# Kernel tuning notes

Measured on AMD Instinct MI355X. Metric: run time of the kernel, lower is better.

Reference implementation:

```python
import jax, jax.numpy as jnp
import numpy as np

N = 50000   # nodes
E = 600000  # edges
D = 128     # input_dim
H = 128     # hidden_dim
K = 2       # num_layers (propagation hops)


def setup_inputs() -> dict:
    key = jax.random.key(0)
    k1, k2, k3 = jax.random.split(key, 3)
    x = jax.random.normal(k1, (N, D), dtype=jnp.float32)
    edge_index = jax.random.randint(k2, (2, E), 0, N, dtype=jnp.int64)
    # Linear(input_dim -> hidden_dim) params (PyG default: glorot-ish weight, zero bias)
    W = jax.random.normal(k3, (H, D), dtype=jnp.float32) / np.float32(np.sqrt(D))
    b = jnp.zeros((H,), dtype=jnp.float32)
    return {"x": x, "edge_index": edge_index, "W": W, "b": b}


def reference(x, edge_index, W, b):
    n = x.shape[0]
    loop = jnp.arange(n, dtype=edge_index.dtype)
    # gcn_norm: add self-loops with weight 1, symmetric normalization
    row = jnp.concatenate([edge_index[0], loop])  # source nodes
    col = jnp.concatenate([edge_index[1], loop])  # target nodes
    w = jnp.ones(row.shape[0], dtype=x.dtype)
    deg = jax.ops.segment_sum(w, col, num_segments=n)
    dinv = jnp.where(deg > 0, jax.lax.rsqrt(deg), jnp.zeros_like(deg))
    norm = dinv[row] * w * dinv[col]  # [E+N]
    # K hops of normalized sparse propagation: x <- A_hat @ x
    for _ in range(K):
        x = jax.ops.segment_sum(norm[:, None] * x[row], col, num_segments=n)
    # Linear projection + activation
    z = x @ W.T + b
    return jax.nn.relu(z)
```

## Files before the change

### kernel.cpp

```cpp
#include <hip/hip_runtime.h>

#define D 128
#define CAP 128
typedef unsigned int uint;
typedef unsigned short ushort;
typedef __attribute__((ext_vector_type(8))) short bf16x8;
typedef __attribute__((ext_vector_type(4))) float f32x4;

__device__ __forceinline__ float2 bf2_to_f2(uint v) {
    union { uint u; float f; } a, b;
    a.u = v << 16;
    b.u = v & 0xffff0000u;
    return make_float2(a.f, b.f);
}
__device__ __forceinline__ uint f2_to_bf2(float x, float y) {
    uint xu = __float_as_uint(x), yu = __float_as_uint(y);
    xu += 0x7fffu + ((xu >> 16) & 1u);
    yu += 0x7fffu + ((yu >> 16) & 1u);
    return (xu >> 16) | (yu & 0xffff0000u);
}

__global__ __launch_bounds__(256) void build_cast_kernel(
        const int* __restrict__ ei, int E, int* __restrict__ deg, int* __restrict__ slots,
        const float* __restrict__ x, uint2* __restrict__ zX, int n,
        const float* __restrict__ W, uint* __restrict__ Wbf,
        int cntB, int xB) {
    int b = blockIdx.x, t = threadIdx.x;
    if (b < cntB) {
        int e = b * 256 + t;
        if (e < E) {
            int r = ei[e];
            int c = ei[E + e];
            int pos = atomicAdd(&deg[c], 1);
            if (pos < CAP) slots[c * CAP + pos] = r;
        }
    } else if (b < cntB + xB) {
        int idx = (b - cntB) * 256 + t;
        if (idx < n * 32) {
            float4 v = ((const float4*)x)[idx];
            uint2 o;
            o.x = f2_to_bf2(v.x, v.y);
            o.y = f2_to_bf2(v.z, v.w);
            zX[idx] = o;
        }
    } else {
        int i = (b - cntB - xB) * 256 + t;
        if (i < (D * D) / 2) {
            float2 wv = ((const float2*)W)[i];
            Wbf[i] = f2_to_bf2(wv.x, wv.y);
        }
    }
}

__global__ __launch_bounds__(256) void prop1_kernel(const uint* __restrict__ zin,
                                                    uint* __restrict__ zout,
                                                    const int* __restrict__ deg,
                                                    const int* __restrict__ slots,
                                                    int n) {
    int wv = threadIdx.x >> 6, lane = threadIdx.x & 63;
    int c = blockIdx.x * 4 + wv;
    if (c >= n) return;
    int len = deg[c]; if (len > CAP) len = CAP;
    const int* lst = slots + c * CAP;
    size_t selfoff = (size_t)c * 64 + lane;
    float dc = rsqrtf((float)(len + 1));
    float2 sf = bf2_to_f2(zin[selfoff]);
    float2 acc = make_float2(sf.x * dc, sf.y * dc);
    int k = 0;
    for (; k + 7 < len; k += 8) {
        int r0 = lst[k],     r1 = lst[k + 1], r2 = lst[k + 2], r3 = lst[k + 3];
        int r4 = lst[k + 4], r5 = lst[k + 5], r6 = lst[k + 6], r7 = lst[k + 7];
        uint v0 = zin[(size_t)r0 * 64 + lane], v1 = zin[(size_t)r1 * 64 + lane];
        uint v2 = zin[(size_t)r2 * 64 + lane], v3 = zin[(size_t)r3 * 64 + lane];
        uint v4 = zin[(size_t)r4 * 64 + lane], v5 = zin[(size_t)r5 * 64 + lane];
        uint v6 = zin[(size_t)r6 * 64 + lane], v7 = zin[(size_t)r7 * 64 + lane];
        float d0 = rsqrtf((float)(deg[r0] + 1)), d1 = rsqrtf((float)(deg[r1] + 1));
        float d2 = rsqrtf((float)(deg[r2] + 1)), d3 = rsqrtf((float)(deg[r3] + 1));
        float d4 = rsqrtf((float)(deg[r4] + 1)), d5 = rsqrtf((float)(deg[r5] + 1));
        float d6 = rsqrtf((float)(deg[r6] + 1)), d7 = rsqrtf((float)(deg[r7] + 1));
        float2 f0 = bf2_to_f2(v0), f1 = bf2_to_f2(v1), f2 = bf2_to_f2(v2), f3 = bf2_to_f2(v3);
        float2 f4 = bf2_to_f2(v4), f5 = bf2_to_f2(v5), f6 = bf2_to_f2(v6), f7 = bf2_to_f2(v7);
        acc.x += (fmaf(d0, f0.x, d1 * f1.x) + fmaf(d2, f2.x, d3 * f3.x))
               + (fmaf(d4, f4.x, d5 * f5.x) + fmaf(d6, f6.x, d7 * f7.x));
        acc.y += (fmaf(d0, f0.y, d1 * f1.y) + fmaf(d2, f2.y, d3 * f3.y))
               + (fmaf(d4, f4.y, d5 * f5.y) + fmaf(d6, f6.y, d7 * f7.y));
    }
    for (; k < len; ++k) {
        int r = lst[k];
        float d = rsqrtf((float)(deg[r] + 1));
        float2 f = bf2_to_f2(zin[(size_t)r * 64 + lane]);
        acc.x = fmaf(d, f.x, acc.x);
        acc.y = fmaf(d, f.y, acc.y);
    }
    float sc = dc * dc;
    zout[selfoff] = f2_to_bf2(acc.x * sc, acc.y * sc);
}

__global__ __launch_bounds__(256) void prop2_kernel(const uint* __restrict__ zin,
                                                    uint* __restrict__ zout,
                                                    const int* __restrict__ deg,
                                                    const int* __restrict__ slots,
                                                    int n) {
    int wv = threadIdx.x >> 6, lane = threadIdx.x & 63;
    int c = blockIdx.x * 4 + wv;
    if (c >= n) return;
    int len = deg[c]; if (len > CAP) len = CAP;
    const int* lst = slots + c * CAP;
    size_t selfoff = (size_t)c * 64 + lane;
    float2 acc = bf2_to_f2(zin[selfoff]);
    int k = 0;
    for (; k + 7 < len; k += 8) {
        int r0 = lst[k],     r1 = lst[k + 1], r2 = lst[k + 2], r3 = lst[k + 3];
        int r4 = lst[k + 4], r5 = lst[k + 5], r6 = lst[k + 6], r7 = lst[k + 7];
        uint v0 = zin[(size_t)r0 * 64 + lane], v1 = zin[(size_t)r1 * 64 + lane];
        uint v2 = zin[(size_t)r2 * 64 + lane], v3 = zin[(size_t)r3 * 64 + lane];
        uint v4 = zin[(size_t)r4 * 64 + lane], v5 = zin[(size_t)r5 * 64 + lane];
        uint v6 = zin[(size_t)r6 * 64 + lane], v7 = zin[(size_t)r7 * 64 + lane];
        float2 f0 = bf2_to_f2(v0), f1 = bf2_to_f2(v1), f2 = bf2_to_f2(v2), f3 = bf2_to_f2(v3);
        float2 f4 = bf2_to_f2(v4), f5 = bf2_to_f2(v5), f6 = bf2_to_f2(v6), f7 = bf2_to_f2(v7);
        acc.x += ((f0.x + f1.x) + (f2.x + f3.x)) + ((f4.x + f5.x) + (f6.x + f7.x));
        acc.y += ((f0.y + f1.y) + (f2.y + f3.y)) + ((f4.y + f5.y) + (f6.y + f7.y));
    }
    for (; k < len; ++k) {
        float2 f = bf2_to_f2(zin[(size_t)lst[k] * 64 + lane]);
        acc.x += f.x; acc.y += f.y;
    }
    float s = rsqrtf((float)(len + 1));
    zout[selfoff] = f2_to_bf2(acc.x * s, acc.y * s);
}

#define GN 64
__global__ __launch_bounds__(256) void gemm_mfma(const uint4* __restrict__ x2,
                                                 const uint4* __restrict__ Wbf,
                                                 const float* __restrict__ bias,
                                                 float* __restrict__ out, int n) {
    __shared__ __align__(16) ushort xs[GN][136];
    __shared__ __align__(16) ushort ws[D][136];
    int t = threadIdx.x;
    int n0 = blockIdx.x * GN;
    for (int i = t; i < D * 16; i += 256) {
        int row = i >> 4, c8 = i & 15;
        uint4 v = Wbf[i];
        *(uint4*)&ws[row][c8 * 8] = v;
    }
    for (int i = t; i < GN * 16; i += 256) {
        int row = i >> 4, c8 = i & 15;
        int node = n0 + row;
        uint4 v = (node < n) ? x2[(size_t)node * 16 + c8] : make_uint4(0u, 0u, 0u, 0u);
        *(uint4*)&xs[row][c8 * 8] = v;
    }
    __syncthreads();

    int w = t >> 6, lane = t & 63;
    int m0 = w * 16;
    int mrow = lane & 15, quad = lane >> 4;

    bf16x8 a[4];
#pragma unroll
    for (int q = 0; q < 4; ++q)
        a[q] = *(const bf16x8*)&xs[m0 + mrow][q * 32 + quad * 8];

    f32x4 acc[8];
#pragma unroll
    for (int ht = 0; ht < 8; ++ht) {
        acc[ht] = (f32x4){0.f, 0.f, 0.f, 0.f};
#pragma unroll
        for (int q = 0; q < 4; ++q) {
            bf16x8 bfr = *(const bf16x8*)&ws[ht * 16 + mrow][q * 32 + quad * 8];
            acc[ht] = __builtin_amdgcn_mfma_f32_16x16x32_bf16(a[q], bfr, acc[ht], 0, 0, 0);
        }
    }

#pragma unroll
    for (int ht = 0; ht < 8; ++ht) {
        int h = ht * 16 + mrow;
        float bv = bias[h];
#pragma unroll
        for (int reg = 0; reg < 4; ++reg) {
            int node = n0 + m0 + quad * 4 + reg;
            if (node < n)
                out[(size_t)node * D + h] = fmaxf(acc[ht][reg] + bv, 0.f);
        }
    }
}

extern "C" void kernel_launch(void* const* d_in, const int* in_sizes, int n_in,
                              void* d_out, int out_size, void* d_ws, size_t ws_size,
                              hipStream_t stream) {
    const float* x  = (const float*)d_in[0];
    const int*   ei = (const int*)d_in[1];
    const float* W  = (const float*)d_in[2];
    const float* bias = (const float*)d_in[3];
    float* out = (float*)d_out;
    int N = in_sizes[0] / D;
    int E = in_sizes[1] / 2;

    char* p = (char*)d_ws;
    auto alloc = [&](size_t bytes) -> void* {
        void* r = p; p += (bytes + 511) & ~(size_t)511; return r;
    };
    int*    deg     = (int*)alloc((size_t)N * 4);
    int*    slots   = (int*)alloc((size_t)N * CAP * 4);
    uint*   zX      = (uint*)alloc((size_t)N * 64 * 4);
    uint*   zB      = (uint*)alloc((size_t)N * 64 * 4);
    uint*   zA      = (uint*)alloc((size_t)N * 64 * 4);
    uint*   Wbf     = (uint*)alloc((size_t)(D * D / 2) * 4);

    int cntB = (E + 255) / 256;
    int xB   = (N * 32 + 255) / 256;
    int wB   = ((D * D / 2) + 255) / 256;

    hipMemsetAsync(deg, 0, (size_t)N * 4, stream);
    build_cast_kernel<<<cntB + xB + wB, 256, 0, stream>>>(ei, E, deg, slots, x, (uint2*)zX, N,
                                                          W, Wbf, cntB, xB);
    prop1_kernel<<<(N + 3) / 4, 256, 0, stream>>>(zX, zB, deg, slots, N);
    prop2_kernel<<<(N + 3) / 4, 256, 0, stream>>>(zB, zA, deg, slots, N);
    gemm_mfma<<<(N + GN - 1) / GN, 256, 0, stream>>>((const uint4*)zA, (const uint4*)Wbf, bias, out, N);
}
```

Measured before the change: 199.3 us.

## Fuse second propagation hop into MFMA GEMM and shrink neighbor slot capacity

The second propagation hop now runs inside the GEMM kernel. Each wave gathers neighbor features for 16 nodes and writes the bf16 result straight into shared memory, so the intermediate feature buffer is never written to or read back from global memory. The weight cast to bf16 moves into each GEMM block, one prop2 launch is removed, and the per-node slot capacity is halved from 128 to 64 to cut the adjacency footprint. The cost is that far fewer waves now do the latency-bound gather, each handling 16 nodes in series with LDS-limited occupancy, which may hide memory latency worse. Every block also redundantly converts the full weight matrix.

```diff
diff --git a/kernel.cpp b/kernel.cpp
--- a/kernel.cpp
+++ b/kernel.cpp
@@ -1,7 +1,7 @@
 #include <hip/hip_runtime.h>
 
 #define D 128
-#define CAP 128
+#define CAP 64
 typedef unsigned int uint;
 typedef unsigned short ushort;
 typedef __attribute__((ext_vector_type(8))) short bf16x8;
@@ -22,9 +22,7 @@
 
 __global__ __launch_bounds__(256) void build_cast_kernel(
         const int* __restrict__ ei, int E, int* __restrict__ deg, int* __restrict__ slots,
-        const float* __restrict__ x, uint2* __restrict__ zX, int n,
-        const float* __restrict__ W, uint* __restrict__ Wbf,
-        int cntB, int xB) {
+        const float* __restrict__ x, uint2* __restrict__ zX, int n, int cntB) {
     int b = blockIdx.x, t = threadIdx.x;
     if (b < cntB) {
         int e = b * 256 + t;
@@ -34,7 +32,7 @@
             int pos = atomicAdd(&deg[c], 1);
             if (pos < CAP) slots[c * CAP + pos] = r;
         }
-    } else if (b < cntB + xB) {
+    } else {
         int idx = (b - cntB) * 256 + t;
         if (idx < n * 32) {
             float4 v = ((const float4*)x)[idx];
@@ -42,12 +40,6 @@
             o.x = f2_to_bf2(v.x, v.y);
             o.y = f2_to_bf2(v.z, v.w);
             zX[idx] = o;
-        }
-    } else {
-        int i = (b - cntB - xB) * 256 + t;
-        if (i < (D * D) / 2) {
-            float2 wv = ((const float2*)W)[i];
-            Wbf[i] = f2_to_bf2(wv.x, wv.y);
         }
     }
 }
@@ -96,62 +88,55 @@
     zout[selfoff] = f2_to_bf2(acc.x * sc, acc.y * sc);
 }
 
-__global__ __launch_bounds__(256) void prop2_kernel(const uint* __restrict__ zin,
-                                                    uint* __restrict__ zout,
-                                                    const int* __restrict__ deg,
-                                                    const int* __restrict__ slots,
-                                                    int n) {
-    int wv = threadIdx.x >> 6, lane = threadIdx.x & 63;
-    int c = blockIdx.x * 4 + wv;
-    if (c >= n) return;
-    int len = deg[c]; if (len > CAP) len = CAP;
-    const int* lst = slots + c * CAP;
-    size_t selfoff = (size_t)c * 64 + lane;
-    float2 acc = bf2_to_f2(zin[selfoff]);
-    int k = 0;
-    for (; k + 7 < len; k += 8) {
-        int r0 = lst[k],     r1 = lst[k + 1], r2 = lst[k + 2], r3 = lst[k + 3];
-        int r4 = lst[k + 4], r5 = lst[k + 5], r6 = lst[k + 6], r7 = lst[k + 7];
-        uint v0 = zin[(size_t)r0 * 64 + lane], v1 = zin[(size_t)r1 * 64 + lane];
-        uint v2 = zin[(size_t)r2 * 64 + lane], v3 = zin[(size_t)r3 * 64 + lane];
-        uint v4 = zin[(size_t)r4 * 64 + lane], v5 = zin[(size_t)r5 * 64 + lane];
-        uint v6 = zin[(size_t)r6 * 64 + lane], v7 = zin[(size_t)r7 * 64 + lane];
-        float2 f0 = bf2_to_f2(v0), f1 = bf2_to_f2(v1), f2 = bf2_to_f2(v2), f3 = bf2_to_f2(v3);
-        float2 f4 = bf2_to_f2(v4), f5 = bf2_to_f2(v5), f6 = bf2_to_f2(v6), f7 = bf2_to_f2(v7);
-        acc.x += ((f0.x + f1.x) + (f2.x + f3.x)) + ((f4.x + f5.x) + (f6.x + f7.x));
-        acc.y += ((f0.y + f1.y) + (f2.y + f3.y)) + ((f4.y + f5.y) + (f6.y + f7.y));
-    }
-    for (; k < len; ++k) {
-        float2 f = bf2_to_f2(zin[(size_t)lst[k] * 64 + lane]);
-        acc.x += f.x; acc.y += f.y;
-    }
-    float s = rsqrtf((float)(len + 1));
-    zout[selfoff] = f2_to_bf2(acc.x * s, acc.y * s);
-}
-
 #define GN 64
-__global__ __launch_bounds__(256) void gemm_mfma(const uint4* __restrict__ x2,
-                                                 const uint4* __restrict__ Wbf,
-                                                 const float* __restrict__ bias,
-                                                 float* __restrict__ out, int n) {
+__global__ __launch_bounds__(256) void prop2_gemm(const uint* __restrict__ zin,
+                                                  const int* __restrict__ deg,
+                                                  const int* __restrict__ slots,
+                                                  const float* __restrict__ W,
+                                                  const float* __restrict__ bias,
+                                                  float* __restrict__ out, int n) {
     __shared__ __align__(16) ushort xs[GN][136];
     __shared__ __align__(16) ushort ws[D][136];
     int t = threadIdx.x;
+    int w = t >> 6, lane = t & 63;
     int n0 = blockIdx.x * GN;
-    for (int i = t; i < D * 16; i += 256) {
-        int row = i >> 4, c8 = i & 15;
-        uint4 v = Wbf[i];
-        *(uint4*)&ws[row][c8 * 8] = v;
+
+    for (int i = t; i < (D * D) / 2; i += 256) {
+        float2 wv = ((const float2*)W)[i];
+        uint u = f2_to_bf2(wv.x, wv.y);
+        int row = i >> 6, col2 = i & 63;
+        *(uint*)&xs[0][0 * 0];
+        *(uint*)&ws[row][col2 * 2] = u;
     }
-    for (int i = t; i < GN * 16; i += 256) {
-        int row = i >> 4, c8 = i & 15;
-        int node = n0 + row;
-        uint4 v = (node < n) ? x2[(size_t)node * 16 + c8] : make_uint4(0u, 0u, 0u, 0u);
-        *(uint4*)&xs[row][c8 * 8] = v;
+
+    for (int i = 0; i < 16; ++i) {
+        int c = n0 + w * 16 + i;
+        if (c >= n) break;
+        int len = deg[c]; if (len > CAP) len = CAP;
+        const int* lst = slots + c * CAP;
+        float2 acc = bf2_to_f2(zin[(size_t)c * 64 + lane]);
+        int k = 0;
+        for (; k + 7 < len; k += 8) {
+            int r0 = lst[k],     r1 = lst[k + 1], r2 = lst[k + 2], r3 = lst[k + 3];
+            int r4 = lst[k + 4], r5 = lst[k + 5], r6 = lst[k + 6], r7 = lst[k + 7];
+            uint v0 = zin[(size_t)r0 * 64 + lane], v1 = zin[(size_t)r1 * 64 + lane];
+            uint v2 = zin[(size_t)r2 * 64 + lane], v3 = zin[(size_t)r3 * 64 + lane];
+            uint v4 = zin[(size_t)r4 * 64 + lane], v5 = zin[(size_t)r5 * 64 + lane];
+            uint v6 = zin[(size_t)r6 * 64 + lane], v7 = zin[(size_t)r7 * 64 + lane];
+            float2 f0 = bf2_to_f2(v0), f1 = bf2_to_f2(v1), f2 = bf2_to_f2(v2), f3 = bf2_to_f2(v3);
+            float2 f4 = bf2_to_f2(v4), f5 = bf2_to_f2(v5), f6 = bf2_to_f2(v6), f7 = bf2_to_f2(v7);
+            acc.x += ((f0.x + f1.x) + (f2.x + f3.x)) + ((f4.x + f5.x) + (f6.x + f7.x));
+            acc.y += ((f0.y + f1.y) + (f2.y + f3.y)) + ((f4.y + f5.y) + (f6.y + f7.y));
+        }
+        for (; k < len; ++k) {
+            float2 f = bf2_to_f2(zin[(size_t)lst[k] * 64 + lane]);
+            acc.x += f.x; acc.y += f.y;
+        }
+        float s = rsqrtf((float)(len + 1));
+        *(uint*)&xs[w * 16 + i][lane * 2] = f2_to_bf2(acc.x * s, acc.y * s);
     }
     __syncthreads();
 
-    int w = t >> 6, lane = t & 63;
     int m0 = w * 16;
     int mrow = lane & 15, quad = lane >> 4;
 
@@ -203,17 +188,12 @@
     int*    slots   = (int*)alloc((size_t)N * CAP * 4);
     uint*   zX      = (uint*)alloc((size_t)N * 64 * 4);
     uint*   zB      = (uint*)alloc((size_t)N * 64 * 4);
-    uint*   zA      = (uint*)alloc((size_t)N * 64 * 4);
-    uint*   Wbf     = (uint*)alloc((size_t)(D * D / 2) * 4);
 
     int cntB = (E + 255) / 256;
     int xB   = (N * 32 + 255) / 256;
-    int wB   = ((D * D / 2) + 255) / 256;
 
     hipMemsetAsync(deg, 0, (size_t)N * 4, stream);
-    build_cast_kernel<<<cntB + xB + wB, 256, 0, stream>>>(ei, E, deg, slots, x, (uint2*)zX, N,
-                                                          W, Wbf, cntB, xB);
+    build_cast_kernel<<<cntB + xB, 256, 0, stream>>>(ei, E, deg, slots, x, (uint2*)zX, N, cntB);
     prop1_kernel<<<(N + 3) / 4, 256, 0, stream>>>(zX, zB, deg, slots, N);
-    prop2_kernel<<<(N + 3) / 4, 256, 0, stream>>>(zB, zA, deg, slots, N);
-    gemm_mfma<<<(N + GN - 1) / GN, 256, 0, stream>>>((const uint4*)zA, (const uint4*)Wbf, bias, out, N);
+    prop2_gemm<<<(N + GN - 1) / GN, 256, 0, stream>>>(zB, deg, slots, W, bias, out, N);
 }
```

Result: slower. 261.4 us (+31.2%).
